# Kernel optimization log

Measured on AMD Instinct MI355X. Metric: run time of the kernel, lower is better.

Reference implementation:

```python
import jax, jax.numpy as jnp
import numpy as np

B, K, M, L = 16, 256, 16, 64
DET_C, HID, H, DEPTH = 1152, 128, 4, 2
DK = HID // H
SCALE = np.float32(1.0 / np.sqrt(DK))


def _ln(x, g, b):
    mu = jnp.mean(x, -1, keepdims=True)
    v = jnp.mean((x - mu) ** 2, -1, keepdims=True)
    return (x - mu) * jax.lax.rsqrt(v + 1e-5) * g + b


def _bn(x, g, b, m, v):  # eval-mode BatchNorm1d, channel-last
    return (x - m) * (g * jax.lax.rsqrt(v + 1e-5)) + b


def _prelu(x, a):
    return jnp.where(x >= 0, x, a * x)


def _mha(q_in, k_in, v_in, Wq, bq, Wk, bk, Wv, bv, Wo, bo, lg, lb, bias=None, mask=None):
    # MultiHeadAttention: scaled dot-product + residual + LayerNorm (eval, no dropout)
    Bb, Nq, _ = q_in.shape
    Nk = k_in.shape[1]
    q = (q_in @ Wq.T + bq).reshape(Bb, Nq, H, DK).transpose(0, 2, 1, 3)
    k = (k_in @ Wk.T + bk).reshape(Bb, Nk, H, DK).transpose(0, 2, 1, 3)
    v = (v_in @ Wv.T + bv).reshape(Bb, Nk, H, DK).transpose(0, 2, 1, 3)
    att = jnp.einsum('bhqd,bhkd->bhqk', q, k) * SCALE
    if bias is not None:
        att = att + bias  # way='add': per-head distance bias
    if mask is not None:
        att = jnp.where(mask, jnp.float32(-1e9), att)
    att = jax.nn.softmax(att, axis=-1)
    out = jnp.einsum('bhqk,bhkd->bhqd', att, v).transpose(0, 2, 1, 3).reshape(Bb, Nq, HID)
    out = out @ Wo.T + bo
    return _ln(q_in + out, lg, lb)


def setup_inputs() -> dict:
    key = jax.random.key(0)
    ks = iter(jax.random.split(key, 64))
    def nrm(shape, s=0.05):
        return jax.random.normal(next(ks), shape, jnp.float32) * s
    d = {}
    d['center'] = jax.random.normal(next(ks), (B, K, 3), jnp.float32)
    d['detr_features'] = nrm((B, K, DET_C), 1.0)
    d['lang_fea'] = nrm((B * M, L, HID), 1.0)
    d['fc_W1'] = nrm((HID, DET_C)); d['fc_b1'] = jnp.zeros((HID,), jnp.float32)
    for pre in ['bn1', 'mbn1', 'mbn2']:
        d[pre + '_g'] = jnp.ones((HID,), jnp.float32)
        d[pre + '_b'] = jnp.zeros((HID,), jnp.float32)
        d[pre + '_m'] = jnp.zeros((HID,), jnp.float32)
        d[pre + '_v'] = jnp.ones((HID,), jnp.float32)
    d['pr1_a'] = 0.25 * jnp.ones((HID,), jnp.float32)
    d['fc_W2'] = nrm((HID, HID)); d['fc_b2'] = jnp.zeros((HID,), jnp.float32)
    for pre in ['sa', 'ca']:
        for nm in ['Wq', 'Wk', 'Wv', 'Wo']:
            d[f'{pre}_{nm}'] = nrm((DEPTH, HID, HID))
        for nm in ['bq', 'bk', 'bv', 'bo', 'lb']:
            d[f'{pre}_{nm}'] = jnp.zeros((DEPTH, HID), jnp.float32)
        d[f'{pre}_lg'] = jnp.ones((DEPTH, HID), jnp.float32)
    d['m_W1'] = nrm((HID, HID)); d['m_b1'] = jnp.zeros((HID,), jnp.float32)
    d['mp1_a'] = 0.25 * jnp.ones((1,), jnp.float32)
    d['m_W2'] = nrm((HID, HID)); d['m_b2'] = jnp.zeros((HID,), jnp.float32)
    d['mp2_a'] = 0.25 * jnp.ones((1,), jnp.float32)
    d['m_W3'] = nrm((1, HID)); d['m_b3'] = jnp.zeros((1,), jnp.float32)
    d['attention_mask'] = jax.random.bernoulli(next(ks), 0.2, (B * M, 1, 1, L))
    d['len_nun_max'] = M
    return d


def reference(center, detr_features, lang_fea,
              fc_W1, fc_b1, bn1_g, bn1_b, bn1_m, bn1_v, pr1_a, fc_W2, fc_b2,
              sa_Wq, sa_bq, sa_Wk, sa_bk, sa_Wv, sa_bv, sa_Wo, sa_bo, sa_lg, sa_lb,
              ca_Wq, ca_bq, ca_Wk, ca_bk, ca_Wv, ca_bv, ca_Wo, ca_bo, ca_lg, ca_lb,
              m_W1, m_b1, mbn1_g, mbn1_b, mbn1_m, mbn1_v, mp1_a,
              m_W2, m_b2, mbn2_g, mbn2_b, mbn2_m, mbn2_v, mp2_a,
              m_W3, m_b3, attention_mask, len_nun_max):
    # distance-based attention bias (detached in the original)
    c = jax.lax.stop_gradient(center)
    dist = jnp.sqrt(jnp.sum((c[:, None, :, :] - c[:, :, None, :]) ** 2, -1))[:, None]  # (B,1,K,K)
    dw = 1.0 / (dist + 0.01)
    dw = dw / jnp.sum(dw, axis=2, keepdims=True)
    zeros = jnp.zeros_like(dw)
    dist_weights = jnp.concatenate([dw, -dist, zeros, zeros], axis=1)  # (B,H,K,K), one bias per head

    # features_concat: Conv1d(1x1) + BN + PReLU + Conv1d(1x1), channel-last
    x = detr_features @ fc_W1.T + fc_b1
    x = _prelu(_bn(x, bn1_g, bn1_b, bn1_m, bn1_v), pr1_a)
    x = x @ fc_W2.T + fc_b2  # (B,K,HID)

    feats = _mha(x, x, x, sa_Wq[0], sa_bq[0], sa_Wk[0], sa_bk[0], sa_Wv[0], sa_bv[0],
                 sa_Wo[0], sa_bo[0], sa_lg[0], sa_lb[0], bias=dist_weights)

    m = int(len_nun_max)
    feats = jnp.broadcast_to(feats[:, None], (B, m, K, HID)).reshape(B * m, K, HID)
    dwb = jnp.broadcast_to(dist_weights[:, None], (B, m, H, K, K)).reshape(B * m, H, K, K)

    f1 = _mha(feats, lang_fea, lang_fea, ca_Wq[0], ca_bq[0], ca_Wk[0], ca_bk[0], ca_Wv[0],
              ca_bv[0], ca_Wo[0], ca_bo[0], ca_lg[0], ca_lb[0], mask=attention_mask)
    for i in range(1, DEPTH):
        f1 = _mha(f1, f1, f1, sa_Wq[i], sa_bq[i], sa_Wk[i], sa_bk[i], sa_Wv[i], sa_bv[i],
                  sa_Wo[i], sa_bo[i], sa_lg[i], sa_lb[i], bias=dwb)
        f1 = _mha(f1, lang_fea, lang_fea, ca_Wq[i], ca_bq[i], ca_Wk[i], ca_bk[i], ca_Wv[i],
                  ca_bv[i], ca_Wo[i], ca_bo[i], ca_lg[i], ca_lb[i], mask=attention_mask)

    # match head: conv1x1+BN+PReLU x2 + conv1x1 -> 1
    y = f1 @ m_W1.T + m_b1
    y = _prelu(_bn(y, mbn1_g, mbn1_b, mbn1_m, mbn1_v), mp1_a)
    y = y @ m_W2.T + m_b2
    y = _prelu(_bn(y, mbn2_g, mbn2_b, mbn2_m, mbn2_v), mp2_a)
    conf = (y @ m_W3.T + m_b3)[..., 0]  # (B*M, K) cluster_ref
    return conf
```

## Files before the change

### kernel.cpp

```cpp
#include <hip/hip_runtime.h>
#include <hip/hip_bf16.h>
#include <cstdio>

#define KQ   256
#define HID  128
typedef unsigned short u16;
#define SCALE_F 0.1767766952966369f

typedef __bf16 bf16x8 __attribute__((ext_vector_type(8)));
typedef short  s16x8  __attribute__((ext_vector_type(8)));
typedef float  f32x4  __attribute__((ext_vector_type(4)));

static __device__ __forceinline__ float bfu(u16 u) {
    return __uint_as_float(((unsigned)u) << 16);
}
static __device__ __forceinline__ u16 f2b(float f) {
    unsigned u = __float_as_uint(f);
    return (u16)((u + 0x7FFFu + ((u >> 16) & 1u)) >> 16);
}
static __device__ __forceinline__ float ldf(const void* p, int i, int f) {
    return f ? ((const float*)p)[i] : bfu(((const u16*)p)[i]);
}
static __device__ __forceinline__ f32x4 mfma16(s16x8 a, s16x8 b, f32x4 c) {
    return __builtin_amdgcn_mfma_f32_16x16x32_bf16(
        __builtin_bit_cast(bf16x8, a), __builtin_bit_cast(bf16x8, b), c, 0, 0, 0);
}

#define OFF_WB     8256
#define OFF_LANGB  237632
#define OFF_ROWS   3383360
#define OFF_FEATSB 3387456
#define OFF_FAB    3649600
#define OFF_QB     7843904
#define OFF_KB     12038208
#define OFF_VB     16232512
#define OFF_MASK   20426816
#define NEEDF      20430912

#define WB_FCW1 0
#define WB_FCW2 147456
#define WB_SAWQ 163840
#define WB_SAWK 196608
#define WB_SAWV 229376
#define WB_SAWO 262144
#define WB_CAWQ 294912
#define WB_CAWK 327680
#define WB_CAWV 360448
#define WB_CAWO 393216
#define WB_MW1  425984
#define WB_MW2  442368

__global__ __launch_bounds__(256) void k_detect(
    const unsigned* __restrict__ onesw, const unsigned* __restrict__ maskw,
    int* __restrict__ flags)
{
    __shared__ int fb;
    if (threadIdx.x == 0) fb = 0;
    __syncthreads();
    int any = 0;
    for (int i = threadIdx.x; i < 4096; i += 256) any |= (maskw[i] > 1u) ? 1 : 0;
    if (any) atomicOr(&fb, 1);
    __syncthreads();
    if (threadIdx.x == 0) {
        flags[0] = (onesw[0] == 0x3F800000u) ? 1 : 0;
        flags[1] = fb;
    }
}

__global__ __launch_bounds__(256) void k_mask_canon(
    const unsigned char* __restrict__ raw, const int* __restrict__ flags,
    unsigned char* __restrict__ mask8)
{
    int i = blockIdx.x*256 + threadIdx.x;
    if (flags[1]) mask8[i] = raw[i] ? 1 : 0;
    else          mask8[i] = (((const unsigned int*)raw)[i] != 0u) ? 1 : 0;
}

struct CvTab {
    const void* src[14];
    unsigned long long dst[14];
    int bstart[15];
};
__global__ __launch_bounds__(256) void k_convAll(
    CvTab t, u16* __restrict__ U, const int* __restrict__ flags)
{
    int b = blockIdx.x;
    int e = 0;
    while (e < 13 && b >= t.bstart[e+1]) ++e;
    long long local = (long long)(b - t.bstart[e])*1024 + threadIdx.x*4;
    u16* dst = U + t.dst[e] + local;
    if (flags[0]) {
        float4 v = *((const float4*)t.src[e] + (local >> 2));
        ushort4 o; o.x = f2b(v.x); o.y = f2b(v.y); o.z = f2b(v.z); o.w = f2b(v.w);
        *(ushort4*)dst = o;
    } else {
        *(ushort4*)dst = *((const ushort4*)t.src[e] + (local >> 2));
    }
}

__global__ __launch_bounds__(256) void k_rowsum(
    const void* __restrict__ center, float* __restrict__ rsinv,
    const int* __restrict__ flags)
{
    int f  = flags[0];
    int bi = blockIdx.x, b = bi >> 8, j = threadIdx.x;
    float cx = ldf(center, bi*3+0, f), cy = ldf(center, bi*3+1, f), cz = ldf(center, bi*3+2, f);
    int pj = (b << 8) + j;
    float px = ldf(center, pj*3+0, f), py = ldf(center, pj*3+1, f), pz = ldf(center, pj*3+2, f);
    float dx = px-cx, dy = py-cy, dz = pz-cz;
    float d  = sqrtf(dx*dx + dy*dy + dz*dz);
    float w  = 1.f/(d + 0.01f);
    float sw = w;
    #pragma unroll
    for (int m = 32; m >= 1; m >>= 1) sw += __shfl_xor(sw, m);
    __shared__ float red[4];
    if ((j & 63) == 0) red[j >> 6] = sw;
    __syncthreads();
    if (j == 0) rsinv[bi] = 1.f / (red[0] + red[1] + red[2] + red[3]);
}

template<int EPI, bool ABCAST, bool RBCAST>
__global__ __launch_bounds__(256) void k_gemm(
    const u16* __restrict__ A, const u16* __restrict__ W, u16* __restrict__ C,
    int Kd, const void* __restrict__ bias,
    const void* __restrict__ bng, const void* __restrict__ bnb,
    const void* __restrict__ bnm, const void* __restrict__ bnv,
    const void* __restrict__ pa,
    const void* __restrict__ lg, const void* __restrict__ lb,
    const u16* __restrict__ resid, const int* __restrict__ flags, int voff)
{
    __shared__ __align__(16) u16 Wl[128*136];
    int f = flags[0];
    int t = threadIdx.x, w = t>>6, lane = t&63, lm = lane&15, q4 = lane>>4;
    int m0 = blockIdx.x*64;
    int arow = m0 + w*16 + lm;
    int grow = ABCAST ? (((arow>>12)<<8)|(arow&255)) : arow;
    const u16* Abase = A + (size_t)grow*Kd;
    f32x4 acc[8];
    #pragma unroll
    for (int nt = 0; nt < 8; ++nt) acc[nt] = f32x4{0.f,0.f,0.f,0.f};
    int sr = t>>1, ss = (t&1)*64;
    for (int k0 = 0; k0 < Kd; k0 += 128) {
        const u16* src = W + (size_t)sr*Kd + k0 + ss;
        u16* dst = Wl + sr*136 + ss;
        #pragma unroll
        for (int i = 0; i < 8; ++i) *(s16x8*)(dst + i*8) = *(const s16x8*)(src + i*8);
        __syncthreads();
        s16x8 aF[4];
        #pragma unroll
        for (int ks = 0; ks < 4; ++ks) aF[ks] = *(const s16x8*)(Abase + k0 + ks*32 + q4*8);
        #pragma unroll
        for (int nt = 0; nt < 8; ++nt)
            #pragma unroll
            for (int ks = 0; ks < 4; ++ks) {
                s16x8 bF = *(const s16x8*)(Wl + (nt*16+lm)*136 + ks*32 + q4*8);
                acc[nt] = mfma16(aF[ks], bF, acc[nt]);
            }
        __syncthreads();
    }
    int row = m0 + w*16 + q4*4;
    if (EPI == 3) {
        float xs[8][4];
        #pragma unroll
        for (int nt = 0; nt < 8; ++nt) {
            int ch = nt*16 + lm;
            float bs = ldf(bias, voff + ch, f);
            #pragma unroll
            for (int r = 0; r < 4; ++r) {
                int rr = row + r;
                int rrow = RBCAST ? (((rr>>12)<<8)|(rr&255)) : rr;
                xs[nt][r] = acc[nt][r] + bs + bfu(resid[(size_t)rrow*HID + ch]);
            }
        }
        #pragma unroll
        for (int r = 0; r < 4; ++r) {
            float sm = 0.f, sq = 0.f;
            #pragma unroll
            for (int nt = 0; nt < 8; ++nt) { sm += xs[nt][r]; sq += xs[nt][r]*xs[nt][r]; }
            #pragma unroll
            for (int d = 1; d <= 8; d <<= 1) { sm += __shfl_xor(sm, d); sq += __shfl_xor(sq, d); }
            float mean = sm * (1.f/128.f);
            float var  = sq * (1.f/128.f) - mean*mean;
            float rs   = rsqrtf(var + 1e-5f);
            #pragma unroll
            for (int nt = 0; nt < 8; ++nt) {
                int ch = nt*16 + lm;
                float g = ldf(lg, voff + ch, f), bb = ldf(lb, voff + ch, f);
                C[(size_t)(row+r)*HID + ch] = f2b((xs[nt][r]-mean)*rs*g + bb);
            }
        }
    } else if (EPI == 4) {
        float sum[4] = {0.f, 0.f, 0.f, 0.f};
        float al = ldf(pa, 0, f);
        #pragma unroll
        for (int nt = 0; nt < 8; ++nt) {
            int ch = nt*16 + lm;
            float bs = ldf(bias, ch, f);
            float g  = ldf(bng, ch, f), bb = ldf(bnb, ch, f);
            float mn = ldf(bnm, ch, f), vv = ldf(bnv, ch, f);
            float scl = g * rsqrtf(vv + 1e-5f);
            float sh  = bb - mn*scl;
            float w3v = ldf(lg, ch, f);
            #pragma unroll
            for (int r = 0; r < 4; ++r) {
                float x = acc[nt][r] + bs;
                x = x*scl + sh;
                x = (x >= 0.f) ? x : al*x;
                sum[r] += x * w3v;
            }
        }
        #pragma unroll
        for (int r = 0; r < 4; ++r)
            #pragma unroll
            for (int d = 1; d <= 8; d <<= 1) sum[r] += __shfl_xor(sum[r], d);
        if (lm == 0) {
            float b3v = ldf(lb, 0, f);
            #pragma unroll
            for (int r = 0; r < 4; ++r) {
                float rr = sum[r] + b3v;
                if (f) ((float*)C)[row + r] = rr;
                else   C[row + r] = f2b(rr);
            }
        }
    } else {
        #pragma unroll
        for (int nt = 0; nt < 8; ++nt) {
            int ch = nt*16 + lm;
            float bs = ldf(bias, voff + ch, f);
            float scl = 1.f, sh = 0.f, al = 0.f;
            if (EPI >= 1) {
                float g  = ldf(bng, ch, f), bb = ldf(bnb, ch, f);
                float mn = ldf(bnm, ch, f), vv = ldf(bnv, ch, f);
                scl = g * rsqrtf(vv + 1e-5f);
                sh  = bb - mn*scl;
                al  = (EPI == 2) ? ldf(pa, 0, f) : ldf(pa, ch, f);
            }
            #pragma unroll
            for (int r = 0; r < 4; ++r) {
                float x = acc[nt][r] + bs;
                if (EPI >= 1) { x = x*scl + sh; x = (x >= 0.f) ? x : al*x; }
                C[(size_t)(row+r)*HID + ch] = f2b(x);
            }
        }
    }
}

template<bool ABCAST>
__global__ __launch_bounds__(256) void k_gemmN(
    const u16* __restrict__ A,
    const u16* __restrict__ W0, const u16* __restrict__ W1, const u16* __restrict__ W2,
    u16* __restrict__ C0, u16* __restrict__ C1, u16* __restrict__ C2,
    const void* __restrict__ b0, const void* __restrict__ b1, const void* __restrict__ b2,
    const int* __restrict__ flags, int voff)
{
    __shared__ __align__(16) u16 Wl[128*136];
    int y = blockIdx.y;
    const u16* W = (y == 0) ? W0 : (y == 1) ? W1 : W2;
    u16* C = (y == 0) ? C0 : (y == 1) ? C1 : C2;
    const void* bias = (y == 0) ? b0 : (y == 1) ? b1 : b2;
    int f = flags[0];
    int t = threadIdx.x, w = t>>6, lane = t&63, lm = lane&15, q4 = lane>>4;
    int m0 = blockIdx.x*64;
    int arow = m0 + w*16 + lm;
    int grow = ABCAST ? (((arow>>12)<<8)|(arow&255)) : arow;
    const u16* Abase = A + (size_t)grow*128;
    f32x4 acc[8];
    #pragma unroll
    for (int nt = 0; nt < 8; ++nt) acc[nt] = f32x4{0.f,0.f,0.f,0.f};
    int sr = t>>1, ss = (t&1)*64;
    {
        const u16* src = W + (size_t)sr*128 + ss;
        u16* dst = Wl + sr*136 + ss;
        #pragma unroll
        for (int i = 0; i < 8; ++i) *(s16x8*)(dst + i*8) = *(const s16x8*)(src + i*8);
    }
    __syncthreads();
    s16x8 aF[4];
    #pragma unroll
    for (int ks = 0; ks < 4; ++ks) aF[ks] = *(const s16x8*)(Abase + ks*32 + q4*8);
    #pragma unroll
    for (int nt = 0; nt < 8; ++nt)
        #pragma unroll
        for (int ks = 0; ks < 4; ++ks) {
            s16x8 bF = *(const s16x8*)(Wl + (nt*16+lm)*136 + ks*32 + q4*8);
            acc[nt] = mfma16(aF[ks], bF, acc[nt]);
        }
    int row = m0 + w*16 + q4*4;
    #pragma unroll
    for (int nt = 0; nt < 8; ++nt) {
        int ch = nt*16 + lm;
        float bs = ldf(bias, voff + ch, f);
        #pragma unroll
        for (int r = 0; r < 4; ++r)
            C[(size_t)(row+r)*HID + ch] = f2b(acc[nt][r] + bs);
    }
}

__global__ __launch_bounds__(256) void k_sattn(
    const u16* __restrict__ Q, const u16* __restrict__ K, const u16* __restrict__ V,
    u16* __restrict__ O, const void* __restrict__ center,
    const float* __restrict__ rsinv, const int* __restrict__ flags, int bdiv)
{
    __shared__ __align__(16) u16 Kl[256*40];
    __shared__ __align__(16) u16 Vt[32*264];
    __shared__ __align__(16) u16 P[4][16*264];
    __shared__ float cxl[256], cyl[256], czl[256], rsl[256];
    int s = blockIdx.x, h = blockIdx.y;
    int t = threadIdx.x, w = t>>6, lane = t&63, lm = lane&15, q4 = lane>>4;
    int f = flags[0];
    int b = s / bdiv;
    {
        const u16* src = K + ((size_t)s*KQ + t)*HID + h*32;
        u16* dst = Kl + t*40;
        #pragma unroll
        for (int i = 0; i < 4; ++i) *(s16x8*)(dst + i*8) = *(const s16x8*)(src + i*8);
    }
    for (int idx = t; idx < 256*8; idx += 256) {
        int k = idx >> 3, d4 = idx & 7;
        ushort4 u = *(const ushort4*)(V + ((size_t)s*KQ + k)*HID + h*32 + d4*4);
        Vt[(d4*4+0)*264 + k] = u.x;
        Vt[(d4*4+1)*264 + k] = u.y;
        Vt[(d4*4+2)*264 + k] = u.z;
        Vt[(d4*4+3)*264 + k] = u.w;
    }
    {
        int j = (b << 8) + t;
        cxl[t] = ldf(center, j*3+0, f);
        cyl[t] = ldf(center, j*3+1, f);
        czl[t] = ldf(center, j*3+2, f);
        rsl[t] = rsinv[j];
    }
    __syncthreads();
    u16* Pw = P[w];
    for (int qt = 0; qt < 4; ++qt) {
        int qrow0 = qt*64 + w*16;
        s16x8 aq = *(const s16x8*)(Q + ((size_t)s*KQ + qrow0 + lm)*HID + h*32 + q4*8);
        float qx[4], qy[4], qz[4];
        if (h < 2) {
            #pragma unroll
            for (int r = 0; r < 4; ++r) {
                int q = qrow0 + q4*4 + r;
                qx[r] = cxl[q]; qy[r] = cyl[q]; qz[r] = czl[q];
            }
        }
        float S[16][4];
        #pragma unroll
        for (int kt = 0; kt < 16; ++kt) {
            s16x8 bF = *(const s16x8*)(Kl + (kt*16+lm)*40 + q4*8);
            f32x4 acc = f32x4{0.f,0.f,0.f,0.f};
            acc = mfma16(aq, bF, acc);
            int key = kt*16 + lm;
            float kx = 0.f, ky = 0.f, kz = 0.f, rs_ = 1.f;
            if (h < 2) { kx = cxl[key]; ky = cyl[key]; kz = czl[key]; rs_ = rsl[key]; }
            #pragma unroll
            for (int r = 0; r < 4; ++r) {
                float sc = acc[r]*SCALE_F;
                if (h < 2) {
                    float dx = qx[r]-kx, dy = qy[r]-ky, dz = qz[r]-kz;
                    float d  = sqrtf(dx*dx + dy*dy + dz*dz);
                    if (h == 0) sc += __builtin_amdgcn_rcpf(d + 0.01f) * rs_;
                    else        sc -= d;
                }
                S[kt][r] = sc;
            }
        }
        float linv[4];
        #pragma unroll
        for (int r = 0; r < 4; ++r) {
            float m = -3.0e38f;
            #pragma unroll
            for (int kt = 0; kt < 16; ++kt) m = fmaxf(m, S[kt][r]);
            #pragma unroll
            for (int d = 1; d <= 8; d <<= 1) m = fmaxf(m, __shfl_xor(m, d));
            float sum = 0.f;
            #pragma unroll
            for (int kt = 0; kt < 16; ++kt) { float p = __expf(S[kt][r]-m); S[kt][r] = p; sum += p; }
            #pragma unroll
            for (int d = 1; d <= 8; d <<= 1) sum += __shfl_xor(sum, d);
            linv[r] = __builtin_amdgcn_rcpf(sum);
        }
        #pragma unroll
        for (int kt = 0; kt < 16; ++kt)
            #pragma unroll
            for (int r = 0; r < 4; ++r)
                Pw[(q4*4+r)*264 + kt*16 + lm] = f2b(S[kt][r]);
        #pragma unroll
        for (int nt = 0; nt < 2; ++nt) {
            f32x4 acc = f32x4{0.f,0.f,0.f,0.f};
            #pragma unroll
            for (int ks = 0; ks < 8; ++ks) {
                s16x8 ap = *(const s16x8*)(Pw + lm*264 + ks*32 + q4*8);
                s16x8 bv = *(const s16x8*)(Vt + (nt*16+lm)*264 + ks*32 + q4*8);
                acc = mfma16(ap, bv, acc);
            }
            #pragma unroll
            for (int r = 0; r < 4; ++r)
                O[((size_t)s*KQ + qrow0 + q4*4 + r)*HID + h*32 + nt*16 + lm] = f2b(acc[r] * linv[r]);
        }
    }
}

__global__ __launch_bounds__(256) void k_xattn(
    const u16* __restrict__ Q, const u16* __restrict__ K, const u16* __restrict__ V,
    u16* __restrict__ O, const unsigned char* __restrict__ mask)
{
    __shared__ __align__(16) u16 Kl[64*40];
    __shared__ __align__(16) u16 Vt[32*72];
    __shared__ __align__(16) u16 P[4][16*72];
    __shared__ float madd[64];
    int s = blockIdx.x, h = blockIdx.y;
    int t = threadIdx.x, w = t>>6, lane = t&63, lm = lane&15, q4 = lane>>4;
    if (t < 64) {
        const u16* src = K + ((size_t)s*64 + t)*HID + h*32;
        u16* dst = Kl + t*40;
        #pragma unroll
        for (int i = 0; i < 4; ++i) *(s16x8*)(dst + i*8) = *(const s16x8*)(src + i*8);
        madd[t] = mask[s*64 + t] ? -1.0e9f : 0.f;
    }
    for (int idx = t; idx < 64*8; idx += 256) {
        int k = idx >> 3, d4 = idx & 7;
        ushort4 u = *(const ushort4*)(V + ((size_t)s*64 + k)*HID + h*32 + d4*4);
        Vt[(d4*4+0)*72 + k] = u.x;
        Vt[(d4*4+1)*72 + k] = u.y;
        Vt[(d4*4+2)*72 + k] = u.z;
        Vt[(d4*4+3)*72 + k] = u.w;
    }
    __syncthreads();
    u16* Pw = P[w];
    for (int qt = 0; qt < 4; ++qt) {
        int qrow0 = qt*64 + w*16;
        s16x8 aq = *(const s16x8*)(Q + ((size_t)s*KQ + qrow0 + lm)*HID + h*32 + q4*8);
        float S[4][4];
        #pragma unroll
        for (int kt = 0; kt < 4; ++kt) {
            s16x8 bF = *(const s16x8*)(Kl + (kt*16+lm)*40 + q4*8);
            f32x4 acc = f32x4{0.f,0.f,0.f,0.f};
            acc = mfma16(aq, bF, acc);
            float ma = madd[kt*16 + lm];
            #pragma unroll
            for (int r = 0; r < 4; ++r) S[kt][r] = acc[r]*SCALE_F + ma;
        }
        float linv[4];
        #pragma unroll
        for (int r = 0; r < 4; ++r) {
            float m = -3.0e38f;
            #pragma unroll
            for (int kt = 0; kt < 4; ++kt) m = fmaxf(m, S[kt][r]);
            #pragma unroll
            for (int d = 1; d <= 8; d <<= 1) m = fmaxf(m, __shfl_xor(m, d));
            float sum = 0.f;
            #pragma unroll
            for (int kt = 0; kt < 4; ++kt) { float p = __expf(S[kt][r]-m); S[kt][r] = p; sum += p; }
            #pragma unroll
            for (int d = 1; d <= 8; d <<= 1) sum += __shfl_xor(sum, d);
            linv[r] = __builtin_amdgcn_rcpf(sum);
        }
        #pragma unroll
        for (int kt = 0; kt < 4; ++kt)
            #pragma unroll
            for (int r = 0; r < 4; ++r)
                Pw[(q4*4+r)*72 + kt*16 + lm] = f2b(S[kt][r]);
        #pragma unroll
        for (int nt = 0; nt < 2; ++nt) {
            f32x4 acc = f32x4{0.f,0.f,0.f,0.f};
            #pragma unroll
            for (int ks = 0; ks < 2; ++ks) {
                s16x8 ap = *(const s16x8*)(Pw + lm*72 + ks*32 + q4*8);
                s16x8 bv = *(const s16x8*)(Vt + (nt*16+lm)*72 + ks*32 + q4*8);
                acc = mfma16(ap, bv, acc);
            }
            #pragma unroll
            for (int r = 0; r < 4; ++r)
                O[((size_t)s*KQ + qrow0 + q4*4 + r)*HID + h*32 + nt*16 + lm] = f2b(acc[r] * linv[r]);
        }
    }
}

extern "C" void kernel_launch(void* const* d_in, const int* in_sizes, int n_in,
                              void* d_out, int out_size, void* d_ws, size_t ws_size,
                              hipStream_t stream)
{
    (void)n_in;
    if (ws_size < (size_t)NEEDF * 4) {
        fprintf(stderr, "kernel_launch: ws too small: have %zu need %zu\n",
                ws_size, (size_t)NEEDF * 4);
        hipMemsetAsync(d_out, 0, (size_t)out_size * 2, stream);
        return;
    }
    float* F = (float*)d_ws;
    u16*   U = (u16*)d_ws;
    int* flags = (int*)d_ws;
    u16* WB     = U + (size_t)OFF_WB*2;
    u16* langb  = U + (size_t)OFF_LANGB*2;
    u16* detrb  = U + (size_t)OFF_KB*2;
    u16* featsb = U + (size_t)OFF_FEATSB*2;
    u16* x2b    = U + (size_t)OFF_FAB*2;
    u16* fAb    = U + (size_t)OFF_FAB*2;
    u16* x1b    = U + (size_t)OFF_VB*2;
    u16* Qb     = U + (size_t)OFF_QB*2;
    u16* Kb     = U + (size_t)OFF_KB*2;
    u16* Vb     = U + (size_t)OFF_VB*2;
    float* rsinv = F + OFF_ROWS;
    unsigned char* mask8 = (unsigned char*)(F + OFF_MASK);

    k_detect<<<1, 256, 0, stream>>>((const unsigned*)d_in[8],
                                    (const unsigned*)d_in[48], flags);
    k_mask_canon<<<64, 256, 0, stream>>>((const unsigned char*)d_in[48], flags, mask8);

    CvTab ct;
    {
        const int idx[14] = {3,18,20,21,22,23,30,31,32,33,40,43,1,2};
        const unsigned long long dst[14] = {
            (unsigned long long)OFF_WB*2 + WB_FCW1, (unsigned long long)OFF_WB*2 + WB_FCW2,
            (unsigned long long)OFF_WB*2 + WB_SAWQ, (unsigned long long)OFF_WB*2 + WB_SAWK,
            (unsigned long long)OFF_WB*2 + WB_SAWV, (unsigned long long)OFF_WB*2 + WB_SAWO,
            (unsigned long long)OFF_WB*2 + WB_CAWQ, (unsigned long long)OFF_WB*2 + WB_CAWK,
            (unsigned long long)OFF_WB*2 + WB_CAWV, (unsigned long long)OFF_WB*2 + WB_CAWO,
            (unsigned long long)OFF_WB*2 + WB_MW1,  (unsigned long long)OFF_WB*2 + WB_MW2,
            (unsigned long long)OFF_KB*2,           (unsigned long long)OFF_LANGB*2 };
        const int bs[15] = {0,144,160,192,224,256,288,320,352,384,416,432,448,5056,7104};
        for (int e = 0; e < 14; ++e) { ct.src[e] = d_in[idx[e]]; ct.dst[e] = dst[e]; }
        for (int e = 0; e < 15; ++e) ct.bstart[e] = bs[e];
    }
    k_convAll<<<7104, 256, 0, stream>>>(ct, U, flags);

    k_rowsum<<<4096, 256, 0, stream>>>(d_in[0], rsinv, flags);

    const void* N0 = nullptr;

    k_gemm<1,false,false><<<64, 256, 0, stream>>>(detrb, WB+WB_FCW1, x1b, 1152,
        d_in[4], d_in[5], d_in[6], d_in[7], d_in[8], d_in[17], N0, N0, nullptr, flags, 0);
    k_gemm<0,false,false><<<64, 256, 0, stream>>>(x1b, WB+WB_FCW2, x2b, 128,
        d_in[19], N0,N0,N0,N0,N0, N0, N0, nullptr, flags, 0);

    k_gemmN<false><<<dim3(64,3), 256, 0, stream>>>(x2b,
        WB+WB_SAWQ, WB+WB_SAWK, WB+WB_SAWV, Qb, Kb, Vb,
        d_in[24], d_in[25], d_in[26], flags, 0);
    k_sattn<<<dim3(16,4), 256, 0, stream>>>(Qb, Kb, Vb, Qb, d_in[0], rsinv, flags, 1);
    k_gemm<3,false,false><<<64, 256, 0, stream>>>(Qb, WB+WB_SAWO, featsb, 128,
        d_in[27], N0,N0,N0,N0,N0, d_in[29], d_in[28], x2b, flags, 0);

    k_gemm<0,true, false><<<1024, 256, 0, stream>>>(featsb, WB+WB_CAWQ, Qb, 128,
        d_in[34], N0,N0,N0,N0,N0, N0, N0, nullptr, flags, 0);
    k_gemmN<false><<<dim3(256,2), 256, 0, stream>>>(langb,
        WB+WB_CAWK, WB+WB_CAWV, nullptr, Kb, Vb, nullptr,
        d_in[35], d_in[36], nullptr, flags, 0);
    k_xattn<<<dim3(256,4), 256, 0, stream>>>(Qb, Kb, Vb, Qb, mask8);
    k_gemm<3,false,true><<<1024, 256, 0, stream>>>(Qb, WB+WB_CAWO, fAb, 128,
        d_in[37], N0,N0,N0,N0,N0, d_in[39], d_in[38], featsb, flags, 0);

    k_gemmN<false><<<dim3(1024,3), 256, 0, stream>>>(fAb,
        WB+WB_SAWQ+16384, WB+WB_SAWK+16384, WB+WB_SAWV+16384, Qb, Kb, Vb,
        d_in[24], d_in[25], d_in[26], flags, 128);
    k_sattn<<<dim3(256,4), 256, 0, stream>>>(Qb, Kb, Vb, Qb, d_in[0], rsinv, flags, 16);
    k_gemm<3,false,false><<<1024, 256, 0, stream>>>(Qb, WB+WB_SAWO+16384, fAb, 128,
        d_in[27], N0,N0,N0,N0,N0, d_in[29], d_in[28], fAb, flags, 128);

    k_gemm<0,false,false><<<1024, 256, 0, stream>>>(fAb, WB+WB_CAWQ+16384, Qb, 128,
        d_in[34], N0,N0,N0,N0,N0, N0, N0, nullptr, flags, 128);
    k_gemmN<false><<<dim3(256,2), 256, 0, stream>>>(langb,
        WB+WB_CAWK+16384, WB+WB_CAWV+16384, nullptr, Kb, Vb, nullptr,
        d_in[35], d_in[36], nullptr, flags, 128);
    k_xattn<<<dim3(256,4), 256, 0, stream>>>(Qb, Kb, Vb, Qb, mask8);
    k_gemm<3,false,false><<<1024, 256, 0, stream>>>(Qb, WB+WB_CAWO+16384, fAb, 128,
        d_in[37], N0,N0,N0,N0,N0, d_in[39], d_in[38], fAb, flags, 128);

    k_gemm<2,false,false><<<1024, 256, 0, stream>>>(fAb, WB+WB_MW1, Qb, 128,
        d_in[41], d_in[9], d_in[10], d_in[11], d_in[12], d_in[42], N0, N0, nullptr, flags, 0);
    k_gemm<4,false,false><<<1024, 256, 0, stream>>>(Qb, WB+WB_MW2, (u16*)d_out, 128,
        d_in[44], d_in[13], d_in[14], d_in[15], d_in[16], d_in[45],
        d_in[46], d_in[47], nullptr, flags, 0);
}
```

Measured before the change: 563.9 us.

## Slim self-attention LDS, stream K from global, split first call across query tiles

The self-attention kernel no longer stages K in shared memory; it reads K fragments straight from global memory. The P buffer shrinks to a 16x32 tile per wave, and P is written and consumed by the PV MFMAs in 32-key chunks. This cuts shared memory per block so more blocks fit per CU. A template parameter lets the first (small-batch) call split its four query tiles across blockIdx.z, so that launch uses four times as many blocks. The trade-off is repeated global (cache) reads of K per query tile and more LDS round trips for P.

```diff
diff --git a/kernel.cpp b/kernel.cpp
--- a/kernel.cpp
+++ b/kernel.cpp
@@ -296,25 +296,19 @@
     }
 }
 
+template<int QTPB>
 __global__ __launch_bounds__(256) void k_sattn(
     const u16* __restrict__ Q, const u16* __restrict__ K, const u16* __restrict__ V,
     u16* __restrict__ O, const void* __restrict__ center,
     const float* __restrict__ rsinv, const int* __restrict__ flags, int bdiv)
 {
-    __shared__ __align__(16) u16 Kl[256*40];
     __shared__ __align__(16) u16 Vt[32*264];
-    __shared__ __align__(16) u16 P[4][16*264];
+    __shared__ __align__(16) u16 P[4][16*40];
     __shared__ float cxl[256], cyl[256], czl[256], rsl[256];
     int s = blockIdx.x, h = blockIdx.y;
     int t = threadIdx.x, w = t>>6, lane = t&63, lm = lane&15, q4 = lane>>4;
     int f = flags[0];
     int b = s / bdiv;
-    {
-        const u16* src = K + ((size_t)s*KQ + t)*HID + h*32;
-        u16* dst = Kl + t*40;
-        #pragma unroll
-        for (int i = 0; i < 4; ++i) *(s16x8*)(dst + i*8) = *(const s16x8*)(src + i*8);
-    }
     for (int idx = t; idx < 256*8; idx += 256) {
         int k = idx >> 3, d4 = idx & 7;
         ushort4 u = *(const ushort4*)(V + ((size_t)s*KQ + k)*HID + h*32 + d4*4);
@@ -332,7 +326,9 @@
     }
     __syncthreads();
     u16* Pw = P[w];
-    for (int qt = 0; qt < 4; ++qt) {
+    const u16* Kbase = K + (size_t)s*KQ*HID + h*32;
+    for (int qi = 0; qi < QTPB; ++qi) {
+        int qt = blockIdx.z*QTPB + qi;
         int qrow0 = qt*64 + w*16;
         s16x8 aq = *(const s16x8*)(Q + ((size_t)s*KQ + qrow0 + lm)*HID + h*32 + q4*8);
         float qx[4], qy[4], qz[4];
@@ -346,7 +342,7 @@
         float S[16][4];
         #pragma unroll
         for (int kt = 0; kt < 16; ++kt) {
-            s16x8 bF = *(const s16x8*)(Kl + (kt*16+lm)*40 + q4*8);
+            s16x8 bF = *(const s16x8*)(Kbase + (size_t)(kt*16 + lm)*HID + q4*8);
             f32x4 acc = f32x4{0.f,0.f,0.f,0.f};
             acc = mfma16(aq, bF, acc);
             int key = kt*16 + lm;
@@ -379,24 +375,28 @@
             for (int d = 1; d <= 8; d <<= 1) sum += __shfl_xor(sum, d);
             linv[r] = __builtin_amdgcn_rcpf(sum);
         }
-        #pragma unroll
-        for (int kt = 0; kt < 16; ++kt)
+        f32x4 acc[2];
+        acc[0] = f32x4{0.f,0.f,0.f,0.f};
+        acc[1] = f32x4{0.f,0.f,0.f,0.f};
+        #pragma unroll
+        for (int ks = 0; ks < 8; ++ks) {
+            #pragma unroll
+            for (int kk = 0; kk < 2; ++kk)
+                #pragma unroll
+                for (int r = 0; r < 4; ++r)
+                    Pw[(q4*4+r)*40 + kk*16 + lm] = f2b(S[ks*2+kk][r]);
+            s16x8 ap = *(const s16x8*)(Pw + lm*40 + q4*8);
+            #pragma unroll
+            for (int nt = 0; nt < 2; ++nt) {
+                s16x8 bv = *(const s16x8*)(Vt + (nt*16+lm)*264 + ks*32 + q4*8);
+                acc[nt] = mfma16(ap, bv, acc[nt]);
+            }
+        }
+        #pragma unroll
+        for (int nt = 0; nt < 2; ++nt)
             #pragma unroll
             for (int r = 0; r < 4; ++r)
-                Pw[(q4*4+r)*264 + kt*16 + lm] = f2b(S[kt][r]);
-        #pragma unroll
-        for (int nt = 0; nt < 2; ++nt) {
-            f32x4 acc = f32x4{0.f,0.f,0.f,0.f};
-            #pragma unroll
-            for (int ks = 0; ks < 8; ++ks) {
-                s16x8 ap = *(const s16x8*)(Pw + lm*264 + ks*32 + q4*8);
-                s16x8 bv = *(const s16x8*)(Vt + (nt*16+lm)*264 + ks*32 + q4*8);
-                acc = mfma16(ap, bv, acc);
-            }
-            #pragma unroll
-            for (int r = 0; r < 4; ++r)
-                O[((size_t)s*KQ + qrow0 + q4*4 + r)*HID + h*32 + nt*16 + lm] = f2b(acc[r] * linv[r]);
-        }
+                O[((size_t)s*KQ + qrow0 + q4*4 + r)*HID + h*32 + nt*16 + lm] = f2b(acc[nt][r] * linv[r]);
     }
 }
 
@@ -536,7 +536,7 @@
     k_gemmN<false><<<dim3(64,3), 256, 0, stream>>>(x2b,
         WB+WB_SAWQ, WB+WB_SAWK, WB+WB_SAWV, Qb, Kb, Vb,
         d_in[24], d_in[25], d_in[26], flags, 0);
-    k_sattn<<<dim3(16,4), 256, 0, stream>>>(Qb, Kb, Vb, Qb, d_in[0], rsinv, flags, 1);
+    k_sattn<1><<<dim3(16,4,4), 256, 0, stream>>>(Qb, Kb, Vb, Qb, d_in[0], rsinv, flags, 1);
     k_gemm<3,false,false><<<64, 256, 0, stream>>>(Qb, WB+WB_SAWO, featsb, 128,
         d_in[27], N0,N0,N0,N0,N0, d_in[29], d_in[28], x2b, flags, 0);
 
@@ -552,7 +552,7 @@
     k_gemmN<false><<<dim3(1024,3), 256, 0, stream>>>(fAb,
         WB+WB_SAWQ+16384, WB+WB_SAWK+16384, WB+WB_SAWV+16384, Qb, Kb, Vb,
         d_in[24], d_in[25], d_in[26], flags, 128);
-    k_sattn<<<dim3(256,4), 256, 0, stream>>>(Qb, Kb, Vb, Qb, d_in[0], rsinv, flags, 16);
+    k_sattn<4><<<dim3(256,4,1), 256, 0, stream>>>(Qb, Kb, Vb, Qb, d_in[0], rsinv, flags, 16);
     k_gemm<3,false,false><<<1024, 256, 0, stream>>>(Qb, WB+WB_SAWO+16384, fAb, 128,
         d_in[27], N0,N0,N0,N0,N0, d_in[29], d_in[28], fAb, flags, 128);
 
```

Result: faster. 506.2 us (-10.2%).
